# Performance work log

Measured on AMD Instinct MI355X. Metric: run time of the kernel, lower is better.

## Reference

```python
import jax, jax.numpy as jnp
import numpy as np

DIM = 4096
N_HEADS = 32
N_KV = 8
HEAD_DIM = DIM // N_HEADS  # 128
ROPE_THETA = 10000.0


def setup_inputs() -> dict:
    key = jax.random.key(0)
    ks = jax.random.split(key, 5)
    B, S = 1, 2048
    x = jax.random.normal(ks[0], (B, S, DIM), jnp.float32)
    wq = jax.random.normal(ks[1], (N_HEADS * HEAD_DIM, DIM), jnp.float32) * 0.02
    wk = jax.random.normal(ks[2], (N_KV * HEAD_DIM, DIM), jnp.float32) * 0.02
    wv = jax.random.normal(ks[3], (N_KV * HEAD_DIM, DIM), jnp.float32) * 0.02
    wo = jax.random.normal(ks[4], (DIM, DIM), jnp.float32) * 0.02
    # precomputed RoPE frequencies: angle[t, i] = t / theta^(2i/head_dim)
    inv_freq = 1.0 / (ROPE_THETA ** (jnp.arange(0, HEAD_DIM, 2, dtype=jnp.float32) / HEAD_DIM))
    t = jnp.arange(S, dtype=jnp.float32)
    angles = jnp.outer(t, inv_freq)  # [S, HEAD_DIM/2]
    return {"x": x, "wq": wq, "wk": wk, "wv": wv, "wo": wo,
            "freqs_cos": jnp.cos(angles), "freqs_sin": jnp.sin(angles)}


def _apply_rope(v, cos, sin):
    # v: [B, S, H, HEAD_DIM]; cos/sin: [S, HEAD_DIM/2]
    # mirrors torch view_as_complex on (..., hd/2, 2): even idx = real, odd idx = imag
    vr = v.reshape(*v.shape[:-1], HEAD_DIM // 2, 2)
    xr, xi = vr[..., 0], vr[..., 1]
    c = cos[None, :, None, :]
    s = sin[None, :, None, :]
    out_r = xr * c - xi * s
    out_i = xr * s + xi * c
    return jnp.stack([out_r, out_i], axis=-1).reshape(v.shape)


def reference(x, wq, wk, wv, wo, freqs_cos, freqs_sin):
    B, S, _ = x.shape
    rep = N_HEADS // N_KV
    q = (x @ wq.T).reshape(B, S, N_HEADS, HEAD_DIM)
    k = (x @ wk.T).reshape(B, S, N_KV, HEAD_DIM)
    v = (x @ wv.T).reshape(B, S, N_KV, HEAD_DIM)
    q = _apply_rope(q, freqs_cos, freqs_sin)
    k = _apply_rope(k, freqs_cos, freqs_sin)
    # native GQA: group query heads per kv head instead of materializing repeated KV
    qg = q.reshape(B, S, N_KV, rep, HEAD_DIM)
    scale = 1.0 / jnp.sqrt(jnp.asarray(HEAD_DIM, jnp.float32))
    scores = jnp.einsum('bqkrd,bskd->bkrqs', qg, k) * scale  # [B, n_kv, rep, S, S]
    causal = jnp.tril(jnp.ones((S, S), bool))
    scores = jnp.where(causal, scores, -jnp.inf)
    probs = jax.nn.softmax(scores, axis=-1)
    out = jnp.einsum('bkrqs,bskd->bqkrd', probs, v).reshape(B, S, DIM)
    return out @ wo.T
```

## Files before the change

### kernel.cpp

```cpp
#include <hip/hip_runtime.h>
#include <cstdint>

typedef __attribute__((ext_vector_type(8))) __bf16 bf16x8;
typedef __attribute__((ext_vector_type(4))) float  f32x4;
typedef __attribute__((ext_vector_type(8))) unsigned short ushort8;

#define DIM 4096
#define SEQ 2048
#define NH  32
#define NKV 8
#define HD  128

__device__ __forceinline__ float b2f(unsigned short u) {
  union { unsigned int i; float f; } v; v.i = ((unsigned int)u) << 16; return v.f;
}
__device__ __forceinline__ unsigned short f2b(float f) {
  union { float f; unsigned int i; } v; v.f = f;
  unsigned int r = v.i + 0x7fffu + ((v.i >> 16) & 1u);
  return (unsigned short)(r >> 16);
}

__device__ __forceinline__ void gl_lds16(const void* g, void* l) {
  __builtin_amdgcn_global_load_lds(
      (const __attribute__((address_space(1))) void*)(uintptr_t)g,
      (__attribute__((address_space(3))) void*)(uintptr_t)l,
      16, 0, 0);
}

__global__ __launch_bounds__(256) void f32_to_bf16(const float* __restrict__ src,
                                                   unsigned short* __restrict__ dst, int n) {
  const int i = (blockIdx.x * 256 + threadIdx.x) * 8;
  if (i >= n) return;
  const float4 a = *(const float4*)(src + i);
  const float4 b = *(const float4*)(src + i + 4);
  ushort8 o;
  o[0] = f2b(a.x); o[1] = f2b(a.y); o[2] = f2b(a.z); o[3] = f2b(a.w);
  o[4] = f2b(b.x); o[5] = f2b(b.y); o[6] = f2b(b.z); o[7] = f2b(b.w);
  *(ushort8*)(dst + i) = o;
}

template <bool OUT_F32>
__global__ __launch_bounds__(256) void gemm_bt(const unsigned short* __restrict__ A,
                                               const unsigned short* __restrict__ B,
                                               void* __restrict__ Cv,
                                               int M, int N, int K) {
  __shared__ __align__(16) unsigned short As[128 * 32];
  __shared__ __align__(16) unsigned short Bs[128 * 32];
  const int n0   = blockIdx.x * 128;
  const int m0   = blockIdx.y * 128;
  const int tid  = threadIdx.x;
  const int w    = tid >> 6;
  const int lane = tid & 63;
  const int quad = lane >> 4;
  const int l15  = lane & 15;
  const int wm   = (w & 1) * 64;
  const int wn   = (w >> 1) * 64;

  const f32x4 fzero = {0.f, 0.f, 0.f, 0.f};
  f32x4 acc[4][4];
#pragma unroll
  for (int i = 0; i < 4; ++i)
#pragma unroll
    for (int j = 0; j < 4; ++j) acc[i][j] = fzero;

  const int srow = lane >> 2;
  const int scol = (lane & 3) * 8;

  for (int k0 = 0; k0 < K; k0 += 32) {
    __syncthreads();
#pragma unroll
    for (int cc = 0; cc < 2; ++cc) {
      const int c   = w * 2 + cc;
      const int row = c * 16 + srow;
      gl_lds16(A + (size_t)(m0 + row) * K + k0 + scol, (char*)As + c * 1024);
      gl_lds16(B + (size_t)(n0 + row) * K + k0 + scol, (char*)Bs + c * 1024);
    }
    __syncthreads();

    bf16x8 af[4], bfr[4];
#pragma unroll
    for (int i = 0; i < 4; ++i) {
      af[i]  = *(const bf16x8*)(As + (wm + i * 16 + l15) * 32 + quad * 8);
      bfr[i] = *(const bf16x8*)(Bs + (wn + i * 16 + l15) * 32 + quad * 8);
    }
#pragma unroll
    for (int i = 0; i < 4; ++i)
#pragma unroll
      for (int j = 0; j < 4; ++j)
        acc[i][j] = __builtin_amdgcn_mfma_f32_16x16x32_bf16(af[i], bfr[j], acc[i][j], 0, 0, 0);
  }

#pragma unroll
  for (int i = 0; i < 4; ++i)
#pragma unroll
    for (int j = 0; j < 4; ++j) {
      const int m = m0 + wm + i * 16 + quad * 4;
      const int n = n0 + wn + j * 16 + l15;
      if (OUT_F32) {
        float* cp = (float*)Cv + (size_t)m * N + n;
#pragma unroll
        for (int r = 0; r < 4; ++r) cp[(size_t)r * N] = acc[i][j][r];
      } else {
        unsigned short* cp = (unsigned short*)Cv + (size_t)m * N + n;
#pragma unroll
        for (int r = 0; r < 4; ++r) cp[(size_t)r * N] = f2b(acc[i][j][r]);
      }
    }
}

template <bool OUT_F32>
__global__ __launch_bounds__(512, 2) void gemm256x192(const unsigned short* __restrict__ A,
                                                      const unsigned short* __restrict__ B,
                                                      void* __restrict__ Cv,
                                                      int M, int N, int K) {
  __shared__ __align__(16) unsigned short As[2][256 * 64];
  __shared__ __align__(16) unsigned short Bs[2][192 * 64];

  const int n0   = blockIdx.x * 192;
  const int m0   = blockIdx.y * 256;
  const int tid  = threadIdx.x;
  const int w    = tid >> 6;
  const int lane = tid & 63;
  const int quad = lane >> 4;
  const int l15  = lane & 15;
  const int wm   = (w >> 2) * 128;
  const int wn   = (w & 3) * 48;

  const int srow = lane >> 3;
  const int sgr  = (lane & 7) ^ srow;
  const unsigned short* aS = A + (size_t)(m0 + srow) * K + sgr * 8;
  const unsigned short* bS = B + (size_t)(n0 + srow) * K + sgr * 8;

  const int gr0 = ((quad)     ^ (l15 & 7)) * 8;
  const int gr1 = ((quad + 4) ^ (l15 & 7)) * 8;

  const f32x4 fzero = {0.f, 0.f, 0.f, 0.f};
  f32x4 acc[8][3];
#pragma unroll
  for (int i = 0; i < 8; ++i)
#pragma unroll
    for (int j = 0; j < 3; ++j) acc[i][j] = fzero;

  const int NT = K >> 6;

#pragma unroll
  for (int i = 0; i < 4; ++i) {
    const int c = w * 4 + i;
    gl_lds16(aS + (size_t)c * 8 * K, (char*)As[0] + c * 1024);
  }
#pragma unroll
  for (int i = 0; i < 3; ++i) {
    const int c = w * 3 + i;
    gl_lds16(bS + (size_t)c * 8 * K, (char*)Bs[0] + c * 1024);
  }

  for (int t = 0; t < NT; ++t) {
    const unsigned short* Ab = As[t & 1] + (wm + l15) * 64;
    const unsigned short* Bb = Bs[t & 1] + (wn + l15) * 64;

    asm volatile("s_waitcnt vmcnt(0) lgkmcnt(0)" ::: "memory");
    __builtin_amdgcn_s_barrier();
    __builtin_amdgcn_sched_barrier(0);

    if (t + 1 < NT) {
      const int koff = (t + 1) * 64;
      unsigned short* Ad = As[(t + 1) & 1];
      unsigned short* Bd = Bs[(t + 1) & 1];
#pragma unroll
      for (int i = 0; i < 4; ++i) {
        const int c = w * 4 + i;
        gl_lds16(aS + (size_t)c * 8 * K + koff, (char*)Ad + c * 1024);
      }
#pragma unroll
      for (int i = 0; i < 3; ++i) {
        const int c = w * 3 + i;
        gl_lds16(bS + (size_t)c * 8 * K + koff, (char*)Bd + c * 1024);
      }
    }

    bf16x8 bfr[3][2];
#pragma unroll
    for (int nf = 0; nf < 3; ++nf) {
      bfr[nf][0] = *(const bf16x8*)(Bb + nf * 1024 + gr0);
      bfr[nf][1] = *(const bf16x8*)(Bb + nf * 1024 + gr1);
    }
#pragma unroll
    for (int mp = 0; mp < 4; ++mp) {
      bf16x8 a0[2], a1[2];
      a0[0] = *(const bf16x8*)(Ab + (mp * 2 + 0) * 1024 + gr0);
      a0[1] = *(const bf16x8*)(Ab + (mp * 2 + 0) * 1024 + gr1);
      a1[0] = *(const bf16x8*)(Ab + (mp * 2 + 1) * 1024 + gr0);
      a1[1] = *(const bf16x8*)(Ab + (mp * 2 + 1) * 1024 + gr1);
      __builtin_amdgcn_s_setprio(1);
#pragma unroll
      for (int ks = 0; ks < 2; ++ks)
#pragma unroll
        for (int nf = 0; nf < 3; ++nf) {
          acc[mp * 2 + 0][nf] = __builtin_amdgcn_mfma_f32_16x16x32_bf16(a0[ks], bfr[nf][ks],
                                                                        acc[mp * 2 + 0][nf], 0, 0, 0);
          acc[mp * 2 + 1][nf] = __builtin_amdgcn_mfma_f32_16x16x32_bf16(a1[ks], bfr[nf][ks],
                                                                        acc[mp * 2 + 1][nf], 0, 0, 0);
        }
      __builtin_amdgcn_s_setprio(0);
    }
  }

#pragma unroll
  for (int mf = 0; mf < 8; ++mf)
#pragma unroll
    for (int nf = 0; nf < 3; ++nf) {
      const int m = m0 + wm + mf * 16 + quad * 4;
      const int n = n0 + wn + nf * 16 + l15;
      if (OUT_F32) {
        float* cp = (float*)Cv + (size_t)m * N + n;
#pragma unroll
        for (int r = 0; r < 4; ++r) cp[(size_t)r * N] = acc[mf][nf][r];
      } else {
        unsigned short* cp = (unsigned short*)Cv + (size_t)m * N + n;
#pragma unroll
        for (int r = 0; r < 4; ++r) cp[(size_t)r * N] = f2b(acc[mf][nf][r]);
      }
    }
}

template <bool OUT_F32>
__global__ __launch_bounds__(512, 2) void gemm128n256(const unsigned short* __restrict__ A,
                                                      const unsigned short* __restrict__ B,
                                                      void* __restrict__ Cv,
                                                      int M, int N, int K) {
  __shared__ __align__(16) unsigned short As[2][128 * 64];
  __shared__ __align__(16) unsigned short Bs[2][256 * 64];

  const int n0   = blockIdx.x * 256;
  const int m0   = blockIdx.y * 128;
  const int tid  = threadIdx.x;
  const int w    = tid >> 6;
  const int lane = tid & 63;
  const int quad = lane >> 4;
  const int l15  = lane & 15;
  const int wm   = (w >> 2) * 64;
  const int wn   = (w & 3) * 64;

  const int srow = lane >> 3;
  const int sgr  = (lane & 7) ^ srow;
  const unsigned short* aS = A + (size_t)(m0 + srow) * K + sgr * 8;
  const unsigned short* bS = B + (size_t)(n0 + srow) * K + sgr * 8;

  const int gr0 = ((quad)     ^ (l15 & 7)) * 8;
  const int gr1 = ((quad + 4) ^ (l15 & 7)) * 8;

  const f32x4 fzero = {0.f, 0.f, 0.f, 0.f};
  f32x4 acc[4][4];
#pragma unroll
  for (int i = 0; i < 4; ++i)
#pragma unroll
    for (int j = 0; j < 4; ++j) acc[i][j] = fzero;

  const int NT = K >> 6;

#pragma unroll
  for (int i = 0; i < 2; ++i) {
    const int c = w * 2 + i;
    gl_lds16(aS + (size_t)c * 8 * K, (char*)As[0] + c * 1024);
  }
#pragma unroll
  for (int i = 0; i < 4; ++i) {
    const int c = w * 4 + i;
    gl_lds16(bS + (size_t)c * 8 * K, (char*)Bs[0] + c * 1024);
  }

  for (int t = 0; t < NT; ++t) {
    const unsigned short* Ab = As[t & 1] + (wm + l15) * 64;
    const unsigned short* Bb = Bs[t & 1] + (wn + l15) * 64;

    asm volatile("s_waitcnt vmcnt(0) lgkmcnt(0)" ::: "memory");
    __builtin_amdgcn_s_barrier();
    __builtin_amdgcn_sched_barrier(0);

    if (t + 1 < NT) {
      const int koff = (t + 1) * 64;
      unsigned short* Ad = As[(t + 1) & 1];
      unsigned short* Bd = Bs[(t + 1) & 1];
#pragma unroll
      for (int i = 0; i < 2; ++i) {
        const int c = w * 2 + i;
        gl_lds16(aS + (size_t)c * 8 * K + koff, (char*)Ad + c * 1024);
      }
#pragma unroll
      for (int i = 0; i < 4; ++i) {
        const int c = w * 4 + i;
        gl_lds16(bS + (size_t)c * 8 * K + koff, (char*)Bd + c * 1024);
      }
    }

    bf16x8 bfr[4][2];
#pragma unroll
    for (int nf = 0; nf < 4; ++nf) {
      bfr[nf][0] = *(const bf16x8*)(Bb + nf * 1024 + gr0);
      bfr[nf][1] = *(const bf16x8*)(Bb + nf * 1024 + gr1);
    }
#pragma unroll
    for (int mp = 0; mp < 2; ++mp) {
      bf16x8 a0[2], a1[2];
      a0[0] = *(const bf16x8*)(Ab + (mp * 2 + 0) * 1024 + gr0);
      a0[1] = *(const bf16x8*)(Ab + (mp * 2 + 0) * 1024 + gr1);
      a1[0] = *(const bf16x8*)(Ab + (mp * 2 + 1) * 1024 + gr0);
      a1[1] = *(const bf16x8*)(Ab + (mp * 2 + 1) * 1024 + gr1);
      __builtin_amdgcn_s_setprio(1);
#pragma unroll
      for (int ks = 0; ks < 2; ++ks)
#pragma unroll
        for (int nf = 0; nf < 4; ++nf) {
          acc[mp * 2 + 0][nf] = __builtin_amdgcn_mfma_f32_16x16x32_bf16(a0[ks], bfr[nf][ks],
                                                                        acc[mp * 2 + 0][nf], 0, 0, 0);
          acc[mp * 2 + 1][nf] = __builtin_amdgcn_mfma_f32_16x16x32_bf16(a1[ks], bfr[nf][ks],
                                                                        acc[mp * 2 + 1][nf], 0, 0, 0);
        }
      __builtin_amdgcn_s_setprio(0);
    }
  }

#pragma unroll
  for (int mf = 0; mf < 4; ++mf)
#pragma unroll
    for (int nf = 0; nf < 4; ++nf) {
      const int m = m0 + wm + mf * 16 + quad * 4;
      const int n = n0 + wn + nf * 16 + l15;
      if (OUT_F32) {
        float* cp = (float*)Cv + (size_t)m * N + n;
#pragma unroll
        for (int r = 0; r < 4; ++r) cp[(size_t)r * N] = acc[mf][nf][r];
      } else {
        unsigned short* cp = (unsigned short*)Cv + (size_t)m * N + n;
#pragma unroll
        for (int r = 0; r < 4; ++r) cp[(size_t)r * N] = f2b(acc[mf][nf][r]);
      }
    }
}

__global__ void rope_kernel(unsigned short* __restrict__ q, int qstride,
                            unsigned short* __restrict__ k, int kstride,
                            const float* __restrict__ Ct, const float* __restrict__ St) {
  const int idx = blockIdx.x * 256 + threadIdx.x;
  const int total = SEQ * (NH * 64 + NKV * 64);
  if (idx >= total) return;
  const int s = idx / 2560;
  const int r = idx - s * 2560;
  unsigned short* base;
  int i;
  if (r < NH * 64) {
    const int h = r >> 6; i = r & 63;
    base = q + (size_t)s * qstride + h * HD + 2 * i;
  } else {
    const int r2 = r - NH * 64; const int h = r2 >> 6; i = r2 & 63;
    base = k + (size_t)s * kstride + h * HD + 2 * i;
  }
  const float c  = Ct[s * 64 + i];
  const float sn = St[s * 64 + i];
  const float xr = b2f(base[0]);
  const float xi = b2f(base[1]);
  base[0] = f2b(xr * c - xi * sn);
  base[1] = f2b(xr * sn + xi * c);
}

__global__ __launch_bounds__(256) void transpose_v(const unsigned short* __restrict__ v,
                                                   int vstride,
                                                   unsigned short* __restrict__ vt) {
  __shared__ unsigned short tile[64][72];
  const int bs = blockIdx.x;
  const int bd = blockIdx.y;
  const int t  = threadIdx.x;
  const int r  = t >> 2;
  const int c0 = (t & 3) * 16;
  const unsigned short* src = v + (size_t)(bs * 64 + r) * vstride + bd * 64 + c0;
#pragma unroll
  for (int i = 0; i < 2; ++i) {
    ushort8 d = *(const ushort8*)(src + i * 8);
#pragma unroll
    for (int e = 0; e < 8; ++e) tile[r][c0 + i * 8 + e] = d[e];
  }
  __syncthreads();
  unsigned short* dst = vt + (size_t)(bd * 64 + r) * SEQ + bs * 64 + c0;
#pragma unroll
  for (int i = 0; i < 2; ++i) {
    ushort8 o;
#pragma unroll
    for (int e = 0; e < 8; ++e) o[e] = tile[c0 + i * 8 + e][r];
    *(ushort8*)(dst + i * 8) = o;
  }
}

__global__ __launch_bounds__(256) void attn_kernel(const unsigned short* __restrict__ Q, int qstride,
                                                   const unsigned short* __restrict__ K, int kstride,
                                                   const unsigned short* __restrict__ VT,
                                                   unsigned short* __restrict__ O) {
  const int bid  = blockIdx.x;
  const int h    = bid & 31;
  const int pr   = bid >> 5;
  const int g    = h >> 2;
  const int tid  = threadIdx.x;
  const int w    = tid >> 6;
  const int lane = tid & 63;
  const int quad = lane >> 4;
  const int l15  = lane & 15;

  __shared__ __align__(16) unsigned short Ks[64 * 128];
  __shared__ __align__(16) unsigned short Vs[128 * 64];
  __shared__ __align__(16) unsigned short Ps[4][32 * 64];

  const float scale = 0.08838834764831845f;
  const f32x4 fzero = {0.f, 0.f, 0.f, 0.f};

  bf16x8 onesf;
#pragma unroll
  for (int e = 0; e < 8; ++e) onesf[e] = (__bf16)1.0f;

  const int ks_row = (lane >> 4);
  const int ks_q   = (lane & 15);
  const int vs_row = (lane >> 3);
  const int vs_q   = (lane & 7) ^ (lane >> 3);

  unsigned short* pw = Ps[w];

  for (int phase = 0; phase < 2; ++phase) {
    const int qt    = phase ? (15 - pr) : pr;
    const int qrow0 = qt * 128 + w * 32;

    bf16x8 qf[2][4];
#pragma unroll
    for (int gq = 0; gq < 2; ++gq) {
      const unsigned short* qb = Q + (size_t)(qrow0 + gq * 16 + l15) * qstride + h * HD + quad * 8;
#pragma unroll
      for (int c = 0; c < 4; ++c) qf[gq][c] = *(const bf16x8*)(qb + c * 32);
    }

    f32x4 oa[2][8];
    f32x4 ls[2];
#pragma unroll
    for (int gq = 0; gq < 2; ++gq) {
      ls[gq] = fzero;
#pragma unroll
      for (int i = 0; i < 8; ++i) oa[gq][i] = fzero;
    }

    const int n_tiles = 2 * qt + 2;

    for (int kt = 0; kt < n_tiles; ++kt) {
      const int kv0 = kt * 64;
      __syncthreads();
#pragma unroll
      for (int cc = 0; cc < 4; ++cc) {
        const int c = w * 4 + cc;
        {
          const int row = c * 4 + ks_row;
          const int qch = ks_q ^ (row & 15);
          gl_lds16(K + (size_t)(kv0 + row) * kstride + g * HD + qch * 8, (char*)Ks + c * 1024);
        }
        {
          const int row = c * 8 + vs_row;
          gl_lds16(VT + (size_t)(g * HD + row) * SEQ + kv0 + vs_q * 8, (char*)Vs + c * 1024);
        }
      }
      __syncthreads();

      f32x4 s[2][4];
#pragma unroll
      for (int gq = 0; gq < 2; ++gq)
#pragma unroll
        for (int ks = 0; ks < 4; ++ks) s[gq][ks] = fzero;
#pragma unroll
      for (int c = 0; c < 4; ++c)
#pragma unroll
        for (int ks = 0; ks < 4; ++ks) {
          const int row = ks * 16 + l15;
          const int p   = (c * 4 + quad) ^ l15;
          bf16x8 kf = *(const bf16x8*)(Ks + row * 128 + p * 8);
          s[0][ks] = __builtin_amdgcn_mfma_f32_16x16x32_bf16(qf[0][c], kf, s[0][ks], 0, 0, 0);
          s[1][ks] = __builtin_amdgcn_mfma_f32_16x16x32_bf16(qf[1][c], kf, s[1][ks], 0, 0, 0);
        }

#pragma unroll
      for (int gq = 0; gq < 2; ++gq)
#pragma unroll
        for (int r = 0; r < 4; ++r) {
          const int qrow = qrow0 + gq * 16 + quad * 4 + r;
          const int prow = gq * 16 + quad * 4 + r;
#pragma unroll
          for (int ks = 0; ks < 4; ++ks) {
            const float ex = __expf(s[gq][ks][r] * scale);
            const float e  = (kv0 + ks * 16 + l15 <= qrow) ? ex : 0.f;
            const int qc = ks * 2 + (l15 >> 3);
            const int p  = qc ^ (prow & 7);
            pw[prow * 64 + p * 8 + (l15 & 7)] = f2b(e);
          }
        }

#pragma unroll
      for (int ki = 0; ki < 2; ++ki) {
        bf16x8 pf[2];
#pragma unroll
        for (int gq = 0; gq < 2; ++gq) {
          const int row = gq * 16 + l15;
          const int p   = (ki * 4 + quad) ^ (l15 & 7);
          pf[gq] = *(const bf16x8*)(pw + row * 64 + p * 8);
        }
        ls[0] = __builtin_amdgcn_mfma_f32_16x16x32_bf16(pf[0], onesf, ls[0], 0, 0, 0);
        ls[1] = __builtin_amdgcn_mfma_f32_16x16x32_bf16(pf[1], onesf, ls[1], 0, 0, 0);
#pragma unroll
        for (int nt = 0; nt < 8; ++nt) {
          const int vrow = nt * 16 + l15;
          const int p    = (ki * 4 + quad) ^ (l15 & 7);
          bf16x8 vf = *(const bf16x8*)(Vs + vrow * 64 + p * 8);
          oa[0][nt] = __builtin_amdgcn_mfma_f32_16x16x32_bf16(pf[0], vf, oa[0][nt], 0, 0, 0);
          oa[1][nt] = __builtin_amdgcn_mfma_f32_16x16x32_bf16(pf[1], vf, oa[1][nt], 0, 0, 0);
        }
      }
    }

#pragma unroll
    for (int gq = 0; gq < 2; ++gq)
#pragma unroll
      for (int r = 0; r < 4; ++r) {
        const float inv = 1.f / ls[gq][r];
        const int qrow = qrow0 + gq * 16 + quad * 4 + r;
        unsigned short* orow = O + (size_t)qrow * DIM + h * HD;
#pragma unroll
        for (int nt = 0; nt < 8; ++nt) orow[nt * 16 + l15] = f2b(oa[gq][nt][r] * inv);
      }
  }
}

extern "C" void kernel_launch(void* const* d_in, const int* in_sizes, int n_in,
                              void* d_out, int out_size, void* d_ws, size_t ws_size,
                              hipStream_t stream) {
  const float* x  = (const float*)d_in[0];
  const float* wq = (const float*)d_in[1];
  const float* wk = (const float*)d_in[2];
  const float* wv = (const float*)d_in[3];
  const float* wo = (const float*)d_in[4];
  const float* fc = (const float*)d_in[5];
  const float* fs = (const float*)d_in[6];
  float* outp = (float*)d_out;

  const dim3 blk(256);
  const size_t M1 = 1024 * 1024;
  const int nx  = SEQ * DIM;
  const int nqw = DIM * DIM;
  const int nkw = NKV * HD * DIM;
  const int total = SEQ * (NH * 64 + NKV * 64);

  const size_t fused_elems = (8 + 24 + 12 + 2 + 8) * M1;

  if (ws_size >= fused_elems * 2) {
    unsigned short* xb   = (unsigned short*)d_ws;
    unsigned short* wbuf = xb   + 8  * M1;
    unsigned short* qkv  = wbuf + 24 * M1;
    unsigned short* vtb  = qkv  + 12 * M1;
    unsigned short* aob  = vtb  + 2  * M1;

    f32_to_bf16<<<dim3(nx  / 2048), blk, 0, stream>>>(x,  xb, nx);
    f32_to_bf16<<<dim3(nqw / 2048), blk, 0, stream>>>(wq, wbuf, nqw);
    f32_to_bf16<<<dim3(nkw / 2048), blk, 0, stream>>>(wk, wbuf + 16 * M1, nkw);
    f32_to_bf16<<<dim3(nkw / 2048), blk, 0, stream>>>(wv, wbuf + 20 * M1, nkw);

    gemm256x192<false><<<dim3(6144 / 192, SEQ / 256), dim3(512), 0, stream>>>(xb, wbuf, qkv,
                                                                              SEQ, 6144, DIM);

    rope_kernel<<<dim3((total + 255) / 256), blk, 0, stream>>>(qkv, 6144, qkv + 4096, 6144, fc, fs);
    transpose_v<<<dim3(SEQ / 64, 1024 / 64), blk, 0, stream>>>(qkv + 5120, 6144, vtb);
    attn_kernel<<<dim3(256), blk, 0, stream>>>(qkv, 6144, qkv + 4096, 6144, vtb, aob);

    f32_to_bf16<<<dim3(nqw / 2048), blk, 0, stream>>>(wo, wbuf, nqw);
    gemm128n256<true><<<dim3(DIM / 256, SEQ / 128), dim3(512), 0, stream>>>(aob, wbuf, outp,
                                                                            SEQ, DIM, DIM);
  } else {
    unsigned short* xb   = (unsigned short*)d_ws;
    unsigned short* wbuf = xb   + 8  * M1;
    unsigned short* qb   = wbuf + 16 * M1;
    unsigned short* kvb  = qb   + 8  * M1;
    unsigned short* vtb  = kvb  + 4  * M1;
    unsigned short* aob  = vtb  + 2  * M1;

    f32_to_bf16<<<dim3(nx  / 2048), blk, 0, stream>>>(x,  xb, nx);
    f32_to_bf16<<<dim3(nqw / 2048), blk, 0, stream>>>(wq, wbuf, nqw);
    gemm128n256<false><<<dim3(DIM / 256, SEQ / 128), dim3(512), 0, stream>>>(xb, wbuf, qb,
                                                                             SEQ, DIM, DIM);

    f32_to_bf16<<<dim3(nkw / 2048), blk, 0, stream>>>(wk, wbuf, nkw);
    f32_to_bf16<<<dim3(nkw / 2048), blk, 0, stream>>>(wv, wbuf + 4 * M1, nkw);
    gemm_bt<false><<<dim3(2048 / 128, SEQ / 128), blk, 0, stream>>>(xb, wbuf, kvb, SEQ, 2048, DIM);

    rope_kernel<<<dim3((total + 255) / 256), blk, 0, stream>>>(qb, 4096, kvb, 2048, fc, fs);
    transpose_v<<<dim3(SEQ / 64, 1024 / 64), blk, 0, stream>>>(kvb + 1024, 2048, vtb);
    attn_kernel<<<dim3(256), blk, 0, stream>>>(qb, 4096, kvb, 2048, vtb, aob);

    f32_to_bf16<<<dim3(nqw / 2048), blk, 0, stream>>>(wo, wbuf, nqw);
    gemm128n256<true><<<dim3(DIM / 256, SEQ / 128), dim3(512), 0, stream>>>(aob, wbuf, outp,
                                                                            SEQ, DIM, DIM);
  }
}
```

Baseline: 460.8 us.

## Split GEMM inner tile into four barrier-synchronized LDS-load/MFMA phases

Both GEMM kernels now split each K-tile into four phases. Each phase loads a subset of A/B fragments from LDS, then runs a block of MFMAs, with s_barrier, lgkmcnt waits and sched_barrier separating the phases. This ping-pong style schedule is meant to keep waves in lockstep so that one wave's LDS reads overlap another wave's MFMA work and register pressure stays lower. It adds several workgroup barriers per K-step, which can stall waves if the phases are unbalanced.

Result: slower. 479.3 us (+4.0%).

```diff
diff --git a/kernel.cpp b/kernel.cpp
--- a/kernel.cpp
+++ b/kernel.cpp
@@ -178,31 +178,73 @@
       }
     }
 
-    bf16x8 bfr[3][2];
-#pragma unroll
-    for (int nf = 0; nf < 3; ++nf) {
-      bfr[nf][0] = *(const bf16x8*)(Bb + nf * 1024 + gr0);
-      bfr[nf][1] = *(const bf16x8*)(Bb + nf * 1024 + gr1);
-    }
-#pragma unroll
-    for (int mp = 0; mp < 4; ++mp) {
-      bf16x8 a0[2], a1[2];
-      a0[0] = *(const bf16x8*)(Ab + (mp * 2 + 0) * 1024 + gr0);
-      a0[1] = *(const bf16x8*)(Ab + (mp * 2 + 0) * 1024 + gr1);
-      a1[0] = *(const bf16x8*)(Ab + (mp * 2 + 1) * 1024 + gr0);
-      a1[1] = *(const bf16x8*)(Ab + (mp * 2 + 1) * 1024 + gr1);
-      __builtin_amdgcn_s_setprio(1);
-#pragma unroll
-      for (int ks = 0; ks < 2; ++ks)
-#pragma unroll
-        for (int nf = 0; nf < 3; ++nf) {
-          acc[mp * 2 + 0][nf] = __builtin_amdgcn_mfma_f32_16x16x32_bf16(a0[ks], bfr[nf][ks],
-                                                                        acc[mp * 2 + 0][nf], 0, 0, 0);
-          acc[mp * 2 + 1][nf] = __builtin_amdgcn_mfma_f32_16x16x32_bf16(a1[ks], bfr[nf][ks],
-                                                                        acc[mp * 2 + 1][nf], 0, 0, 0);
-        }
-      __builtin_amdgcn_s_setprio(0);
-    }
+    bf16x8 b0[3];
+#pragma unroll
+    for (int nf = 0; nf < 3; ++nf) b0[nf] = *(const bf16x8*)(Bb + nf * 1024 + gr0);
+    bf16x8 a0[4];
+#pragma unroll
+    for (int mf = 0; mf < 4; ++mf) a0[mf] = *(const bf16x8*)(Ab + mf * 1024 + gr0);
+    __builtin_amdgcn_s_barrier();
+    asm volatile("s_waitcnt lgkmcnt(0)" ::: "memory");
+    __builtin_amdgcn_sched_barrier(0);
+    __builtin_amdgcn_s_setprio(1);
+#pragma unroll
+    for (int mf = 0; mf < 4; ++mf)
+#pragma unroll
+      for (int nf = 0; nf < 3; ++nf)
+        acc[mf][nf] = __builtin_amdgcn_mfma_f32_16x16x32_bf16(a0[mf], b0[nf], acc[mf][nf], 0, 0, 0);
+    __builtin_amdgcn_s_setprio(0);
+    __builtin_amdgcn_s_barrier();
+    __builtin_amdgcn_sched_barrier(0);
+
+    bf16x8 a1[4];
+#pragma unroll
+    for (int mf = 0; mf < 4; ++mf) a1[mf] = *(const bf16x8*)(Ab + (4 + mf) * 1024 + gr0);
+    __builtin_amdgcn_s_barrier();
+    asm volatile("s_waitcnt lgkmcnt(0)" ::: "memory");
+    __builtin_amdgcn_sched_barrier(0);
+    __builtin_amdgcn_s_setprio(1);
+#pragma unroll
+    for (int mf = 0; mf < 4; ++mf)
+#pragma unroll
+      for (int nf = 0; nf < 3; ++nf)
+        acc[4 + mf][nf] = __builtin_amdgcn_mfma_f32_16x16x32_bf16(a1[mf], b0[nf], acc[4 + mf][nf], 0, 0, 0);
+    __builtin_amdgcn_s_setprio(0);
+    __builtin_amdgcn_s_barrier();
+    __builtin_amdgcn_sched_barrier(0);
+
+    bf16x8 b1[3];
+#pragma unroll
+    for (int nf = 0; nf < 3; ++nf) b1[nf] = *(const bf16x8*)(Bb + nf * 1024 + gr1);
+    bf16x8 a2[4];
+#pragma unroll
+    for (int mf = 0; mf < 4; ++mf) a2[mf] = *(const bf16x8*)(Ab + mf * 1024 + gr1);
+    __builtin_amdgcn_s_barrier();
+    asm volatile("s_waitcnt lgkmcnt(0)" ::: "memory");
+    __builtin_amdgcn_sched_barrier(0);
+    __builtin_amdgcn_s_setprio(1);
+#pragma unroll
+    for (int mf = 0; mf < 4; ++mf)
+#pragma unroll
+      for (int nf = 0; nf < 3; ++nf)
+        acc[mf][nf] = __builtin_amdgcn_mfma_f32_16x16x32_bf16(a2[mf], b1[nf], acc[mf][nf], 0, 0, 0);
+    __builtin_amdgcn_s_setprio(0);
+    __builtin_amdgcn_s_barrier();
+    __builtin_amdgcn_sched_barrier(0);
+
+    bf16x8 a3[4];
+#pragma unroll
+    for (int mf = 0; mf < 4; ++mf) a3[mf] = *(const bf16x8*)(Ab + (4 + mf) * 1024 + gr1);
+    __builtin_amdgcn_s_barrier();
+    asm volatile("s_waitcnt lgkmcnt(0)" ::: "memory");
+    __builtin_amdgcn_sched_barrier(0);
+    __builtin_amdgcn_s_setprio(1);
+#pragma unroll
+    for (int mf = 0; mf < 4; ++mf)
+#pragma unroll
+      for (int nf = 0; nf < 3; ++nf)
+        acc[4 + mf][nf] = __builtin_amdgcn_mfma_f32_16x16x32_bf16(a3[mf], b1[nf], acc[4 + mf][nf], 0, 0, 0);
+    __builtin_amdgcn_s_setprio(0);
   }
 
 #pragma unroll
@@ -293,31 +335,73 @@
       }
     }
 
-    bf16x8 bfr[4][2];
-#pragma unroll
-    for (int nf = 0; nf < 4; ++nf) {
-      bfr[nf][0] = *(const bf16x8*)(Bb + nf * 1024 + gr0);
-      bfr[nf][1] = *(const bf16x8*)(Bb + nf * 1024 + gr1);
-    }
-#pragma unroll
-    for (int mp = 0; mp < 2; ++mp) {
-      bf16x8 a0[2], a1[2];
-      a0[0] = *(const bf16x8*)(Ab + (mp * 2 + 0) * 1024 + gr0);
-      a0[1] = *(const bf16x8*)(Ab + (mp * 2 + 0) * 1024 + gr1);
-      a1[0] = *(const bf16x8*)(Ab + (mp * 2 + 1) * 1024 + gr0);
-      a1[1] = *(const bf16x8*)(Ab + (mp * 2 + 1) * 1024 + gr1);
-      __builtin_amdgcn_s_setprio(1);
-#pragma unroll
-      for (int ks = 0; ks < 2; ++ks)
-#pragma unroll
-        for (int nf = 0; nf < 4; ++nf) {
-          acc[mp * 2 + 0][nf] = __builtin_amdgcn_mfma_f32_16x16x32_bf16(a0[ks], bfr[nf][ks],
-                                                                        acc[mp * 2 + 0][nf], 0, 0, 0);
-          acc[mp * 2 + 1][nf] = __builtin_amdgcn_mfma_f32_16x16x32_bf16(a1[ks], bfr[nf][ks],
-                                                                        acc[mp * 2 + 1][nf], 0, 0, 0);
-        }
-      __builtin_amdgcn_s_setprio(0);
-    }
+    bf16x8 b0[4];
+#pragma unroll
+    for (int nf = 0; nf < 4; ++nf) b0[nf] = *(const bf16x8*)(Bb + nf * 1024 + gr0);
+    bf16x8 a0[2];
+#pragma unroll
+    for (int mf = 0; mf < 2; ++mf) a0[mf] = *(const bf16x8*)(Ab + mf * 1024 + gr0);
+    __builtin_amdgcn_s_barrier();
+    asm volatile("s_waitcnt lgkmcnt(0)" ::: "memory");
+    __builtin_amdgcn_sched_barrier(0);
+    __builtin_amdgcn_s_setprio(1);
+#pragma unroll
+    for (int mf = 0; mf < 2; ++mf)
+#pragma unroll
+      for (int nf = 0; nf < 4; ++nf)
+        acc[mf][nf] = __builtin_amdgcn_mfma_f32_16x16x32_bf16(a0[mf], b0[nf], acc[mf][nf], 0, 0, 0);
+    __builtin_amdgcn_s_setprio(0);
+    __builtin_amdgcn_s_barrier();
+    __builtin_amdgcn_sched_barrier(0);
+
+    bf16x8 a1[2];
+#pragma unroll
+    for (int mf = 0; mf < 2; ++mf) a1[mf] = *(const bf16x8*)(Ab + (2 + mf) * 1024 + gr0);
+    __builtin_amdgcn_s_barrier();
+    asm volatile("s_waitcnt lgkmcnt(0)" ::: "memory");
+    __builtin_amdgcn_sched_barrier(0);
+    __builtin_amdgcn_s_setprio(1);
+#pragma unroll
+    for (int mf = 0; mf < 2; ++mf)
+#pragma unroll
+      for (int nf = 0; nf < 4; ++nf)
+        acc[2 + mf][nf] = __builtin_amdgcn_mfma_f32_16x16x32_bf16(a1[mf], b0[nf], acc[2 + mf][nf], 0, 0, 0);
+    __builtin_amdgcn_s_setprio(0);
+    __builtin_amdgcn_s_barrier();
+    __builtin_amdgcn_sched_barrier(0);
+
+    bf16x8 b1[4];
+#pragma unroll
+    for (int nf = 0; nf < 4; ++nf) b1[nf] = *(const bf16x8*)(Bb + nf * 1024 + gr1);
+    bf16x8 a2[2];
+#pragma unroll
+    for (int mf = 0; mf < 2; ++mf) a2[mf] = *(const bf16x8*)(Ab + mf * 1024 + gr1);
+    __builtin_amdgcn_s_barrier();
+    asm volatile("s_waitcnt lgkmcnt(0)" ::: "memory");
+    __builtin_amdgcn_sched_barrier(0);
+    __builtin_amdgcn_s_setprio(1);
+#pragma unroll
+    for (int mf = 0; mf < 2; ++mf)
+#pragma unroll
+      for (int nf = 0; nf < 4; ++nf)
+        acc[mf][nf] = __builtin_amdgcn_mfma_f32_16x16x32_bf16(a2[mf], b1[nf], acc[mf][nf], 0, 0, 0);
+    __builtin_amdgcn_s_setprio(0);
+    __builtin_amdgcn_s_barrier();
+    __builtin_amdgcn_sched_barrier(0);
+
+    bf16x8 a3[2];
+#pragma unroll
+    for (int mf = 0; mf < 2; ++mf) a3[mf] = *(const bf16x8*)(Ab + (2 + mf) * 1024 + gr1);
+    __builtin_amdgcn_s_barrier();
+    asm volatile("s_waitcnt lgkmcnt(0)" ::: "memory");
+    __builtin_amdgcn_sched_barrier(0);
+    __builtin_amdgcn_s_setprio(1);
+#pragma unroll
+    for (int mf = 0; mf < 2; ++mf)
+#pragma unroll
+      for (int nf = 0; nf < 4; ++nf)
+        acc[2 + mf][nf] = __builtin_amdgcn_mfma_f32_16x16x32_bf16(a3[mf], b1[nf], acc[2 + mf][nf], 0, 0, 0);
+    __builtin_amdgcn_s_setprio(0);
   }
 
 #pragma unroll
```
